# Kernel tuning notes

Measured on AMD Instinct MI355X. Metric: run time of the kernel, lower is better.

Reference implementation:

```python
import jax, jax.numpy as jnp
import numpy as np

D_MODEL = 1024
N_HEADS = 16
D_HEAD = D_MODEL // N_HEADS
MEM_SIZE = 256


def setup_inputs() -> dict:
    key = jax.random.key(0)
    k_x, k_q, k_o, k_mk, k_mv = jax.random.split(key, 5)
    B, T = 4, 4096
    x = jax.random.normal(k_x, (B, T, D_MODEL), dtype=jnp.float32)
    # xavier_uniform for square Linear weights: bound = sqrt(6/(fan_in+fan_out))
    bound = float(np.sqrt(6.0 / (D_MODEL + D_MODEL)))
    Wq = jax.random.uniform(k_q, (D_MODEL, D_MODEL), minval=-bound, maxval=bound, dtype=jnp.float32)
    Wo = jax.random.uniform(k_o, (D_MODEL, D_MODEL), minval=-bound, maxval=bound, dtype=jnp.float32)
    # kaiming_uniform(a=sqrt(5)) on (H,S,D): fan_in = S*D (last two dims), bound = sqrt(6/((1+a^2)*fan_in)) = 1/sqrt(fan_in)
    bk = float(1.0 / np.sqrt(MEM_SIZE * D_HEAD))
    M_k = jax.random.uniform(k_mk, (N_HEADS, MEM_SIZE, D_HEAD), minval=-bk, maxval=bk, dtype=jnp.float32)
    M_v = jax.random.uniform(k_mv, (N_HEADS, MEM_SIZE, D_HEAD), minval=-0.01, maxval=0.01, dtype=jnp.float32)
    return {"x": x, "Wq": Wq, "Wo": Wo, "M_k": M_k, "M_v": M_v}


def reference(x, Wq, Wo, M_k, M_v):
    B, T, _ = x.shape
    H, S, D = N_HEADS, MEM_SIZE, D_HEAD
    # Q projection (torch Linear: x @ W^T) -> (B, H, T, D)
    Q = (x @ Wq.T).reshape(B, T, H, D).transpose(0, 2, 1, 3)
    scale = D ** -0.5
    # (B, H, T, S) attention against shared external keys
    attn = jnp.einsum("bhtd,hsd->bhts", Q, M_k) * scale
    attn = jax.nn.softmax(attn, axis=-1)
    # double normalization: L1 over the token (T) axis
    attn = attn / (attn.sum(axis=-2, keepdims=True) + 1e-6)
    # dropout = 0.0 (inference): no-op
    out = jnp.einsum("bhts,hsd->bhtd", attn, M_v)
    out = out.transpose(0, 2, 1, 3).reshape(B, T, H * D)
    return out @ Wo.T
```

## Files before the change

kernel.cpp:

```cpp
#include <hip/hip_runtime.h>
#include <math.h>

constexpr int B_  = 4;
constexpr int T_  = 4096;
constexpr int DM_ = 1024;
constexpr int H_  = 16;
constexpr int S_  = 256;
constexpr int BT_ = B_ * T_;
constexpr int NBLK_ = 16;
constexpr size_t QELEMS = (size_t)BT_ * DM_;

typedef _Float16 v8h __attribute__((ext_vector_type(8)));
typedef _Float16 v4h __attribute__((ext_vector_type(4)));
typedef float    v4f __attribute__((ext_vector_type(4)));

__device__ _Float16 g_AH[QELEMS];
__device__ _Float16 g_QH[QELEMS];
__device__ _Float16 g_WqH[DM_ * DM_];
__device__ _Float16 g_WoH[DM_ * DM_];
__device__ _Float16 g_MkH[H_ * S_ * 64];
__device__ _Float16 g_MvT[H_ * 64 * S_];
__device__ _Float16 g_Mv2[(size_t)B_ * H_ * 64 * S_];
__device__ _Float16 g_P[(size_t)B_ * H_ * T_ * S_];
__device__ float    g_cpart[(size_t)B_ * H_ * NBLK_ * S_];
__device__ float    g_colsum_inv[B_ * H_ * S_];

__global__ __launch_bounds__(256) void cvt_h(const float* __restrict__ src,
                                             _Float16* __restrict__ dst,
                                             float scale) {
  const size_t i = (size_t)blockIdx.x * 256 + threadIdx.x;
  const float4* s = (const float4*)src;
  float4 a = s[2 * i], b = s[2 * i + 1];
  v8h o;
  o[0] = (_Float16)(a.x * scale); o[1] = (_Float16)(a.y * scale);
  o[2] = (_Float16)(a.z * scale); o[3] = (_Float16)(a.w * scale);
  o[4] = (_Float16)(b.x * scale); o[5] = (_Float16)(b.y * scale);
  o[6] = (_Float16)(b.z * scale); o[7] = (_Float16)(b.w * scale);
  *(v8h*)&dst[8 * i] = o;
}

__global__ __launch_bounds__(256) void transpose_mv(const float* __restrict__ Mv) {
  const int idx = blockIdx.x * 256 + threadIdx.x;
  const int h = idx >> 14, rem = idx & 16383;
  const int s = rem >> 6, d = rem & 63;
  g_MvT[h * 16384 + d * 256 + s] = (_Float16)Mv[idx];
}

template <typename OUT_T>
__device__ __forceinline__ void gemm_body(const _Float16* __restrict__ Ah,
                                          const _Float16* __restrict__ Wh,
                                          OUT_T* __restrict__ C, float scale) {
  __shared__ _Float16 As[128][72];
  __shared__ _Float16 Bs[128][72];
  const int tid  = threadIdx.x;
  const int m0   = blockIdx.x * 128;
  const int n0   = blockIdx.y * 128;
  const int wid  = tid >> 6;
  const int wm   = wid & 1;
  const int wn   = wid >> 1;
  const int lane = tid & 63;
  const int l15  = lane & 15;
  const int quad = lane >> 4;

  v4f acc[4][4] = {};

  for (int k0 = 0; k0 < 1024; k0 += 64) {
#pragma unroll
    for (int i = 0; i < 4; ++i) {
      int c  = i * 256 + tid;
      int r  = c >> 3;
      int ch = (c & 7) * 8;
      *(v8h*)&As[r][ch] = *(const v8h*)&Ah[(size_t)(m0 + r) * 1024 + k0 + ch];
      *(v8h*)&Bs[r][ch] = *(const v8h*)&Wh[(size_t)(n0 + r) * 1024 + k0 + ch];
    }
    __syncthreads();
#pragma unroll
    for (int kk = 0; kk < 2; ++kk) {
      v8h af[4], bf[4];
#pragma unroll
      for (int i = 0; i < 4; ++i)
        af[i] = *(const v8h*)&As[wm * 64 + i * 16 + l15][kk * 32 + quad * 8];
#pragma unroll
      for (int j = 0; j < 4; ++j)
        bf[j] = *(const v8h*)&Bs[wn * 64 + j * 16 + l15][kk * 32 + quad * 8];
#pragma unroll
      for (int i = 0; i < 4; ++i)
#pragma unroll
        for (int j = 0; j < 4; ++j)
          acc[i][j] = __builtin_amdgcn_mfma_f32_16x16x32_f16(af[i], bf[j], acc[i][j], 0, 0, 0);
    }
    __syncthreads();
  }
#pragma unroll
  for (int i = 0; i < 4; ++i) {
    const size_t mrow = (size_t)(m0 + wm * 64 + i * 16 + quad * 4);
#pragma unroll
    for (int j = 0; j < 4; ++j) {
      const int ncol = n0 + wn * 64 + j * 16 + l15;
#pragma unroll
      for (int r = 0; r < 4; ++r)
        C[(mrow + r) * 1024 + ncol] = (OUT_T)(acc[i][j][r] * scale);
    }
  }
}

__global__ __launch_bounds__(256) void gemm_q16(const _Float16* __restrict__ Wq) {
  gemm_body<_Float16>(g_AH, Wq, g_QH, 1.0f);
}
__global__ __launch_bounds__(256) void gemm_o(const _Float16* __restrict__ Wo,
                                              float* __restrict__ out) {
  gemm_body<float>(g_AH, Wo, out, 1.0f / 512.0f);
}

__global__ __launch_bounds__(256, 2) void attn_p1() {
  __shared__ __align__(16) _Float16 MkS_buf[S_ * 64];
  __shared__ __align__(16) _Float16 Psh[4][16][280];
  __shared__ float csum_sh[4][256];
  const int tid  = threadIdx.x;
  const int bh   = blockIdx.x;
  const int b    = bh >> 4, h = bh & 15;
  const int tblk = blockIdx.y;
  const int wid  = tid >> 6;
  const int lane = tid & 63;
  const int l15  = lane & 15;
  const int quad = lane >> 4;
  char* MkS = (char*)MkS_buf;

  const int tw = tblk * 256 + wid * 64;
  const _Float16* qbase = &g_QH[(size_t)(b * T_ + tw) * 1024 + h * 64];
  v8h afq[4][2];
#pragma unroll
  for (int g = 0; g < 4; ++g) {
    afq[g][0] = *(const v8h*)&qbase[(size_t)(g * 16 + l15) * 1024 + quad * 8];
    afq[g][1] = *(const v8h*)&qbase[(size_t)(g * 16 + l15) * 1024 + 32 + quad * 8];
  }

  {
    const _Float16* mkrow = &g_MkH[h * (S_ * 64) + tid * 64];
#pragma unroll
    for (int c = 0; c < 8; ++c) {
      v8h v = *(const v8h*)&mkrow[c * 8];
      *(v8h*)(MkS + tid * 128 + ((c ^ (tid & 7)) << 4)) = v;
    }
  }

  float csloc[16];
#pragma unroll
  for (int i = 0; i < 16; ++i) csloc[i] = 0.0f;

  __syncthreads();

  for (int g = 0; g < 4; ++g) {
    v4f acc[16] = {};
#pragma unroll
    for (int st = 0; st < 16; ++st) {
      const int row = st * 16 + l15;
      const int sw  = row & 7;
      v8h b0 = *(const v8h*)(MkS + row * 128 + ((quad ^ sw) << 4));
      v8h b1 = *(const v8h*)(MkS + row * 128 + (((4 + quad) ^ sw) << 4));
      acc[st] = __builtin_amdgcn_mfma_f32_16x16x32_f16(afq[g][0], b0, acc[st], 0, 0, 0);
      acc[st] = __builtin_amdgcn_mfma_f32_16x16x32_f16(afq[g][1], b1, acc[st], 0, 0, 0);
    }

#pragma unroll
    for (int r = 0; r < 4; ++r) {
      float ssum = 0.0f;
#pragma unroll
      for (int st = 0; st < 16; ++st) {
        float p = __expf(acc[st][r]);
        acc[st][r] = p; ssum += p;
      }
      ssum += __shfl_xor(ssum, 1); ssum += __shfl_xor(ssum, 2);
      ssum += __shfl_xor(ssum, 4); ssum += __shfl_xor(ssum, 8);
      const float inv = 1.0f / ssum;
#pragma unroll
      for (int st = 0; st < 16; ++st) acc[st][r] *= inv;
    }

#pragma unroll
    for (int st = 0; st < 16; ++st)
      csloc[st] += acc[st][0] + acc[st][1] + acc[st][2] + acc[st][3];

#pragma unroll
    for (int st = 0; st < 16; ++st)
#pragma unroll
      for (int r = 0; r < 4; ++r)
        Psh[wid][quad * 4 + r][st * 16 + l15] = (_Float16)acc[st][r];
    asm volatile("s_waitcnt lgkmcnt(0)" ::: "memory");

    {
      const int tok = tw + g * 16 + l15;
      _Float16* prow = &g_P[((size_t)bh * T_ + tok) * 256];
#pragma unroll
      for (int j = 0; j < 8; ++j) {
        const int ch = j * 4 + quad;
        *(v8h*)&prow[ch * 8] = *(const v8h*)&Psh[wid][l15][ch * 8];
      }
    }
    asm volatile("s_waitcnt lgkmcnt(0)" ::: "memory");
  }

#pragma unroll
  for (int st = 0; st < 16; ++st) {
    float c = csloc[st];
    c += __shfl_xor(c, 16);
    c += __shfl_xor(c, 32);
    if (quad == 0) csum_sh[wid][st * 16 + l15] = c;
  }
  __syncthreads();
  g_cpart[((size_t)bh * NBLK_ + tblk) * 256 + tid] =
      csum_sh[0][tid] + csum_sh[1][tid] + csum_sh[2][tid] + csum_sh[3][tid];
}

__global__ __launch_bounds__(256) void reduce_colsum() {
  const int bh = blockIdx.x;
  const int s  = threadIdx.x;
  float acc = 0.0f;
#pragma unroll
  for (int k = 0; k < NBLK_; ++k)
    acc += g_cpart[((size_t)bh * NBLK_ + k) * 256 + s];
  g_colsum_inv[bh * 256 + s] = 1.0f / (acc + 1e-6f);
}

__global__ __launch_bounds__(256) void scale_mv() {
  const int i8  = blockIdx.x * 256 + threadIdx.x;
  const int bhd = i8 >> 5;
  const int sc  = (i8 & 31) * 8;
  const int h   = (bhd >> 6) & 15;
  const int d   = bhd & 63;
  const int bh  = bhd >> 6;
  v8h mv = *(const v8h*)&g_MvT[(h * 64 + d) * 256 + sc];
  const float* cinv = &g_colsum_inv[bh * 256 + sc];
  v8h o;
#pragma unroll
  for (int j = 0; j < 8; ++j) o[j] = (_Float16)((float)mv[j] * cinv[j]);
  *(v8h*)&g_Mv2[(size_t)bhd * 256 + sc] = o;
}

__global__ __launch_bounds__(256, 2) void pv2() {
  const int tid  = threadIdx.x;
  const int bh   = blockIdx.x;
  const int b    = bh >> 4, h = bh & 15;
  const int gblk = blockIdx.y;
  const int wid  = tid >> 6;
  const int lane = tid & 63;
  const int l15  = lane & 15;
  const int quad = lane >> 4;

  const _Float16* mv2 = &g_Mv2[(size_t)bh * 16384];
  v8h af[4][8];
#pragma unroll
  for (int nt = 0; nt < 4; ++nt)
#pragma unroll
    for (int kc = 0; kc < 8; ++kc)
      af[nt][kc] = *(const v8h*)&mv2[(nt * 16 + l15) * 256 + kc * 32 + quad * 8];

  const int t0w = gblk * 512 + wid * 128;
  const _Float16* pbase = &g_P[((size_t)bh * T_ + t0w) * 256];
  _Float16* obase = &g_AH[((size_t)(b * T_ + t0w)) * 1024 + h * 64];

  v8h bf[8];
#pragma unroll
  for (int kc = 0; kc < 8; ++kc)
    bf[kc] = *(const v8h*)&pbase[(size_t)l15 * 256 + kc * 32 + quad * 8];

  for (int g = 0; g < 8; ++g) {
    v8h nbf[8];
    if (g < 7) {
#pragma unroll
      for (int kc = 0; kc < 8; ++kc)
        nbf[kc] = *(const v8h*)&pbase[(size_t)((g + 1) * 16 + l15) * 256 + kc * 32 + quad * 8];
    }
    v4f acc[4] = {};
#pragma unroll
    for (int kc = 0; kc < 8; ++kc)
#pragma unroll
      for (int nt = 0; nt < 4; ++nt)
        acc[nt] = __builtin_amdgcn_mfma_f32_16x16x32_f16(af[nt][kc], bf[kc], acc[nt], 0, 0, 0);

    _Float16* orow = &obase[(size_t)(g * 16 + l15) * 1024 + quad * 4];
#pragma unroll
    for (int nt = 0; nt < 4; ++nt) {
      v4h o;
#pragma unroll
      for (int r = 0; r < 4; ++r) o[r] = (_Float16)(acc[nt][r] * 512.0f);
      *(v4h*)&orow[nt * 16] = o;
    }
    if (g < 7) {
#pragma unroll
      for (int kc = 0; kc < 8; ++kc) bf[kc] = nbf[kc];
    }
  }
}

extern "C" void kernel_launch(void* const* d_in, const int* in_sizes, int n_in,
                              void* d_out, int out_size, void* d_ws, size_t ws_size,
                              hipStream_t stream) {
  const float* x  = (const float*)d_in[0];
  const float* Wq = (const float*)d_in[1];
  const float* Wo = (const float*)d_in[2];
  const float* Mk = (const float*)d_in[3];
  const float* Mv = (const float*)d_in[4];
  float* out = (float*)d_out;

  _Float16 *AH, *WqH, *WoH, *MkH;
  (void)hipGetSymbolAddress((void**)&AH,  HIP_SYMBOL(g_AH));
  (void)hipGetSymbolAddress((void**)&WqH, HIP_SYMBOL(g_WqH));
  (void)hipGetSymbolAddress((void**)&WoH, HIP_SYMBOL(g_WoH));
  (void)hipGetSymbolAddress((void**)&MkH, HIP_SYMBOL(g_MkH));

  cvt_h<<<8192, 256, 0, stream>>>(x,  AH, 1.0f);
  cvt_h<<<512,  256, 0, stream>>>(Wq, WqH, 1.0f);
  cvt_h<<<512,  256, 0, stream>>>(Wo, WoH, 1.0f);
  cvt_h<<<128,  256, 0, stream>>>(Mk, MkH, 0.125f);
  transpose_mv<<<1024, 256, 0, stream>>>(Mv);
  gemm_q16<<<dim3(BT_ / 128, DM_ / 128), 256, 0, stream>>>(WqH);
  attn_p1<<<dim3(B_ * H_, NBLK_), 256, 0, stream>>>();
  reduce_colsum<<<dim3(B_ * H_), 256, 0, stream>>>();
  scale_mv<<<512, 256, 0, stream>>>();
  pv2<<<dim3(B_ * H_, 8), 256, 0, stream>>>();
  gemm_o<<<dim3(BT_ / 128, DM_ / 128), 256, 0, stream>>>(WoH, out);
}
```

Before: 417.5 us.

## Raise attn_p1 occupancy by dropping LDS staging and prefetching Q per group

The attention-probability kernel no longer stages P tiles and column sums in shared memory. It writes P straight from MFMA accumulators to global memory as scattered 2-byte stores, and writes per-wave partial column sums that reduce_colsum now sums over 64 entries. Q fragments are loaded one group ahead instead of all upfront, which cuts register pressure, and launch bounds are raised to 4 blocks per SM. The risk is that the uncoalesced fp16 global stores of the 32 MB P matrix cost more than the LDS round-trip they replace.

After: 508.3 us. 21.8% more time.

```diff
diff --git a/kernel.cpp b/kernel.cpp
--- a/kernel.cpp
+++ b/kernel.cpp
@@ -22,7 +22,7 @@
 __device__ _Float16 g_MvT[H_ * 64 * S_];
 __device__ _Float16 g_Mv2[(size_t)B_ * H_ * 64 * S_];
 __device__ _Float16 g_P[(size_t)B_ * H_ * T_ * S_];
-__device__ float    g_cpart[(size_t)B_ * H_ * NBLK_ * S_];
+__device__ float    g_cpart[(size_t)B_ * H_ * NBLK_ * 4 * S_];
 __device__ float    g_colsum_inv[B_ * H_ * S_];
 
 __global__ __launch_bounds__(256) void cvt_h(const float* __restrict__ src,
@@ -112,10 +112,8 @@
   gemm_body<float>(g_AH, Wo, out, 1.0f / 512.0f);
 }
 
-__global__ __launch_bounds__(256, 2) void attn_p1() {
+__global__ __launch_bounds__(256, 4) void attn_p1() {
   __shared__ __align__(16) _Float16 MkS_buf[S_ * 64];
-  __shared__ __align__(16) _Float16 Psh[4][16][280];
-  __shared__ float csum_sh[4][256];
   const int tid  = threadIdx.x;
   const int bh   = blockIdx.x;
   const int b    = bh >> 4, h = bh & 15;
@@ -127,13 +125,10 @@
   char* MkS = (char*)MkS_buf;
 
   const int tw = tblk * 256 + wid * 64;
-  const _Float16* qbase = &g_QH[(size_t)(b * T_ + tw) * 1024 + h * 64];
-  v8h afq[4][2];
-#pragma unroll
-  for (int g = 0; g < 4; ++g) {
-    afq[g][0] = *(const v8h*)&qbase[(size_t)(g * 16 + l15) * 1024 + quad * 8];
-    afq[g][1] = *(const v8h*)&qbase[(size_t)(g * 16 + l15) * 1024 + 32 + quad * 8];
-  }
+  const _Float16* qbase = &g_QH[(size_t)(b * T_ + tw) * 1024 + h * 64 + quad * 8];
+
+  v8h a0 = *(const v8h*)&qbase[(size_t)l15 * 1024];
+  v8h a1 = *(const v8h*)&qbase[(size_t)l15 * 1024 + 32];
 
   {
     const _Float16* mkrow = &g_MkH[h * (S_ * 64) + tid * 64];
@@ -150,7 +145,14 @@
 
   __syncthreads();
 
+#pragma unroll 1
   for (int g = 0; g < 4; ++g) {
+    v8h n0, n1;
+    if (g < 3) {
+      n0 = *(const v8h*)&qbase[(size_t)((g + 1) * 16 + l15) * 1024];
+      n1 = *(const v8h*)&qbase[(size_t)((g + 1) * 16 + l15) * 1024 + 32];
+    }
+
     v4f acc[16] = {};
 #pragma unroll
     for (int st = 0; st < 16; ++st) {
@@ -158,8 +160,8 @@
       const int sw  = row & 7;
       v8h b0 = *(const v8h*)(MkS + row * 128 + ((quad ^ sw) << 4));
       v8h b1 = *(const v8h*)(MkS + row * 128 + (((4 + quad) ^ sw) << 4));
-      acc[st] = __builtin_amdgcn_mfma_f32_16x16x32_f16(afq[g][0], b0, acc[st], 0, 0, 0);
-      acc[st] = __builtin_amdgcn_mfma_f32_16x16x32_f16(afq[g][1], b1, acc[st], 0, 0, 0);
+      acc[st] = __builtin_amdgcn_mfma_f32_16x16x32_f16(a0, b0, acc[st], 0, 0, 0);
+      acc[st] = __builtin_amdgcn_mfma_f32_16x16x32_f16(a1, b1, acc[st], 0, 0, 0);
     }
 
 #pragma unroll
@@ -181,23 +183,16 @@
     for (int st = 0; st < 16; ++st)
       csloc[st] += acc[st][0] + acc[st][1] + acc[st][2] + acc[st][3];
 
-#pragma unroll
-    for (int st = 0; st < 16; ++st)
-#pragma unroll
-      for (int r = 0; r < 4; ++r)
-        Psh[wid][quad * 4 + r][st * 16 + l15] = (_Float16)acc[st][r];
-    asm volatile("s_waitcnt lgkmcnt(0)" ::: "memory");
-
     {
-      const int tok = tw + g * 16 + l15;
-      _Float16* prow = &g_P[((size_t)bh * T_ + tok) * 256];
-#pragma unroll
-      for (int j = 0; j < 8; ++j) {
-        const int ch = j * 4 + quad;
-        *(v8h*)&prow[ch * 8] = *(const v8h*)&Psh[wid][l15][ch * 8];
-      }
-    }
-    asm volatile("s_waitcnt lgkmcnt(0)" ::: "memory");
+      _Float16* pg = &g_P[((size_t)bh * T_ + tw + g * 16 + quad * 4) * 256 + l15];
+#pragma unroll
+      for (int st = 0; st < 16; ++st)
+#pragma unroll
+        for (int r = 0; r < 4; ++r)
+          pg[r * 256 + st * 16] = (_Float16)acc[st][r];
+    }
+
+    if (g < 3) { a0 = n0; a1 = n1; }
   }
 
 #pragma unroll
@@ -205,20 +200,22 @@
     float c = csloc[st];
     c += __shfl_xor(c, 16);
     c += __shfl_xor(c, 32);
-    if (quad == 0) csum_sh[wid][st * 16 + l15] = c;
-  }
-  __syncthreads();
-  g_cpart[((size_t)bh * NBLK_ + tblk) * 256 + tid] =
-      csum_sh[0][tid] + csum_sh[1][tid] + csum_sh[2][tid] + csum_sh[3][tid];
+    csloc[st] = c;
+  }
+  if (quad == 0) {
+    float* cp = &g_cpart[(((size_t)bh * NBLK_ + tblk) * 4 + wid) * 256 + l15];
+#pragma unroll
+    for (int st = 0; st < 16; ++st) cp[st * 16] = csloc[st];
+  }
 }
 
 __global__ __launch_bounds__(256) void reduce_colsum() {
   const int bh = blockIdx.x;
   const int s  = threadIdx.x;
   float acc = 0.0f;
-#pragma unroll
-  for (int k = 0; k < NBLK_; ++k)
-    acc += g_cpart[((size_t)bh * NBLK_ + k) * 256 + s];
+#pragma unroll 8
+  for (int k = 0; k < NBLK_ * 4; ++k)
+    acc += g_cpart[((size_t)bh * 64 + k) * 256 + s];
   g_colsum_inv[bh * 256 + s] = 1.0f / (acc + 1e-6f);
 }
 
```
